# Optimization experiments

Measured on AMD Instinct MI355X. Metric: run time of the kernel, lower is better.

Reference implementation:

```python
import jax, jax.numpy as jnp
import numpy as np

B, S, I, H, L = 64, 1024, 512, 512, 2


def setup_inputs() -> dict:
    key = jax.random.key(0)
    ks = jax.random.split(key, 9)
    stdv = 1.0 / np.sqrt(H)
    u = lambda k, shape: jax.random.uniform(k, shape, jnp.float32, -stdv, stdv)
    return {
        "x": jax.random.normal(ks[0], (B, S, I), jnp.float32),
        "w_ih0": u(ks[1], (3 * H, I)),
        "w_hh0": u(ks[2], (3 * H, H)),
        "b_ih0": u(ks[3], (3 * H,)),
        "b_hh0": u(ks[4], (3 * H,)),
        "w_ih1": u(ks[5], (3 * H, H)),
        "w_hh1": u(ks[6], (3 * H, H)),
        "b_ih1": u(ks[7], (3 * H,)),
        "b_hh1": u(ks[8], (3 * H,)),
    }


def _gru_layer(x_seq, w_ih, w_hh, b_ih, b_hh):
    """x_seq: [S, B, I]. Returns (hs [S, B, H], h_last [B, H])."""
    h = w_hh.shape[1]
    # Precompute all input-to-hidden gate pre-activations in one big GEMM.
    gx_seq = jnp.einsum('sbi,gi->sbg', x_seq, w_ih) + b_ih  # [S, B, 3H]

    def step(h_prev, gx):
        gh = h_prev @ w_hh.T + b_hh  # [B, 3H]
        xr, xz, xn = jnp.split(gx, 3, axis=-1)
        hr, hz, hn = jnp.split(gh, 3, axis=-1)
        r = jax.nn.sigmoid(xr + hr)
        z = jax.nn.sigmoid(xz + hz)
        n = jnp.tanh(xn + r * hn)
        h_new = (1.0 - z) * n + z * h_prev
        return h_new, h_new

    h0 = jnp.zeros((x_seq.shape[1], h), x_seq.dtype)
    h_last, hs = jax.lax.scan(step, h0, gx_seq)
    return hs, h_last


def reference(x, w_ih0, w_hh0, b_ih0, b_hh0, w_ih1, w_hh1, b_ih1, b_hh1):
    xs = jnp.transpose(x, (1, 0, 2))  # [S, B, I] (batch_first -> time-major)
    hs0, h_last0 = _gru_layer(xs, w_ih0, w_hh0, b_ih0, b_hh0)
    hs1, h_last1 = _gru_layer(hs0, w_ih1, w_hh1, b_ih1, b_hh1)
    output = jnp.transpose(hs1, (1, 0, 2))  # [B, S, H]
    h_n = jnp.stack([h_last0, h_last1], axis=0)  # [L, B, H]
    return output, h_n
```

## Files before the change

### kernel.cpp

```cpp
#include <hip/hip_runtime.h>
#include <hip/hip_bf16.h>
#include <cstddef>

typedef __attribute__((ext_vector_type(8))) short bf16x8;
typedef __attribute__((ext_vector_type(4))) float f32x4;
typedef __attribute__((ext_vector_type(4))) unsigned int u32x4;

constexpr int kB = 64;
constexpr int kS = 1024;
constexpr int kH = 512;
constexpr int kNBG = 4;
constexpr int kNUG = 32;
constexpr int kHst = 520;
constexpr unsigned kDone4 = 0x01010101u;
constexpr int kSpinCap = 1 << 16;

__device__ __forceinline__ unsigned short f2bf(float f) {
  unsigned int u = __float_as_uint(f);
  u += 0x7FFFu + ((u >> 16) & 1u);
  return (unsigned short)(u >> 16);
}

__device__ __forceinline__ void st_u32_coh(unsigned int* p, unsigned int v) {
  asm volatile("global_store_dword %0, %1, off sc0 sc1" ::"v"(p), "v"(v) : "memory");
}
__device__ __forceinline__ void st_u64_coh(void* p, unsigned long long v) {
  asm volatile("global_store_dwordx2 %0, %1, off sc0 sc1" ::"v"(p), "v"(v) : "memory");
}
__device__ __forceinline__ void st_flag_release8(unsigned char* p, unsigned int v) {
  asm volatile("s_waitcnt vmcnt(0)\n\tglobal_store_byte %0, %1, off sc0 sc1"
               ::"v"(p), "v"(v) : "memory");
}

#define COH_LD16(dst, p, OFF)                                             \
  asm volatile("global_load_dwordx4 %0, %1, off offset:" #OFF " sc0 sc1"  \
               : "=v"(dst) : "v"(p) : "memory")

__device__ __forceinline__ void wait_vm0(void) {
  asm volatile("s_waitcnt vmcnt(0)" ::: "memory");
  __builtin_amdgcn_sched_barrier(0);
}

__device__ __forceinline__ int poll32(const unsigned char* p) {
  for (int i = 0; i < kSpinCap; ++i) {
    u32x4 a, b;
    asm volatile(
        "global_load_dwordx4 %0, %2, off sc0 sc1\n\t"
        "global_load_dwordx4 %1, %2, off offset:16 sc0 sc1\n\t"
        "s_waitcnt vmcnt(0)"
        : "=v"(a), "=v"(b) : "v"(p) : "memory");
    if (a[0] == kDone4 && a[1] == kDone4 && a[2] == kDone4 && a[3] == kDone4 &&
        b[0] == kDone4 && b[1] == kDone4 && b[2] == kDone4 && b[3] == kDone4)
      return 1;
  }
  return 0;
}

__global__ void init_coh(unsigned int* __restrict__ zbase, int n) {
  int i = blockIdx.x * blockDim.x + threadIdx.x;
  if (i < n) st_u32_coh(zbase + i, 0u);
}

__global__ void cvt_f32_bf16(const float* __restrict__ in,
                             unsigned short* __restrict__ out, int n4) {
  int i = blockIdx.x * blockDim.x + threadIdx.x;
  if (i >= n4) return;
  float4 v = ((const float4*)in)[i];
  ushort4 o;
  o.x = f2bf(v.x); o.y = f2bf(v.y); o.z = f2bf(v.z); o.w = f2bf(v.w);
  ((ushort4*)out)[i] = o;
}

__global__ void cvt_x_t(const float* __restrict__ in,
                        unsigned short* __restrict__ out, int n4) {
  int i4 = blockIdx.x * blockDim.x + threadIdx.x;
  if (i4 >= n4) return;
  int d = i4 * 4;
  int i = d & (kH - 1);
  int rem = d / kH;
  int b = rem & (kB - 1);
  int s = rem / kB;
  float4 v = *(const float4*)(in + ((size_t)b * kS + s) * kH + i);
  ushort4 o;
  o.x = f2bf(v.x); o.y = f2bf(v.y); o.z = f2bf(v.z); o.w = f2bf(v.w);
  *(ushort4*)(out + (size_t)d) = o;
}

__launch_bounds__(256, 1)
__global__ void gru_fused(const unsigned short* __restrict__ xbf,
                          const unsigned short* __restrict__ wih0,
                          const unsigned short* __restrict__ whh0,
                          const unsigned short* __restrict__ wih1,
                          const unsigned short* __restrict__ whh1,
                          const float* __restrict__ bih0, const float* __restrict__ bhh0,
                          const float* __restrict__ bih1, const float* __restrict__ bhh1,
                          unsigned short* __restrict__ hs0,
                          unsigned short* __restrict__ h1buf,
                          unsigned char* __restrict__ f0,
                          unsigned char* __restrict__ f1,
                          float* __restrict__ out) {
  const int tid  = threadIdx.x;
  const int lane = tid & 63;
  const int wv   = tid >> 6;
  const int wgid = blockIdx.x;
  const int layer = wgid >> 7;
  const int bg    = wgid & 3;
  const int ug    = (wgid & 127) >> 2;
  const int bgb0  = bg * 16;
  const int j0w   = ug * 16 + wv * 4;

  const unsigned short* wih = layer ? wih1 : wih0;
  const unsigned short* whh = layer ? whh1 : whh0;
  const float* bih = layer ? bih1 : bih0;
  const float* bhh = layer ? bhh1 : bhh0;

  bf16x8 bx[16], bh[16];
  {
    const int n = lane & 15, hi = lane >> 4;
    if (n < 12) {
      const int orig = (n >> 2) * kH + j0w + (n & 3);
      const unsigned short* pX = wih + (size_t)orig * kH + hi * 8;
      const unsigned short* pH = whh + (size_t)orig * kH + hi * 8;
#pragma unroll
      for (int kk = 0; kk < 16; ++kk) {
        bx[kk] = *(const bf16x8*)(pX + kk * 32);
        bh[kk] = *(const bf16x8*)(pH + kk * 32);
      }
    } else {
      bf16x8 z = {0, 0, 0, 0, 0, 0, 0, 0};
#pragma unroll
      for (int kk = 0; kk < 16; ++kk) { bx[kk] = z; bh[kk] = z; }
    }
  }

  const int gb  = tid & 15;
  const int guu = tid >> 4;
  const int unit = ug * 16 + guu;
  const float bihr = bih[unit], bihz = bih[kH + unit], bihn = bih[2 * kH + unit];
  const float bhhr = bhh[unit], bhhz = bhh[kH + unit], bhhn = bhh[2 * kH + unit];
  float hprev = 0.0f;

  __shared__ unsigned short hA[16][kHst];
  __shared__ unsigned short hX[16][kHst];
  __shared__ float gxl[16][52];
  __shared__ float ghl[16][52];
  __shared__ unsigned short hl[16][20];
  __shared__ float hlf[16][20];

  const int n_  = lane & 15;
  const int ahi = (lane >> 4) * 8;
  const int srow  = lane & 15;
  const int scol0 = wv * 128 + (lane >> 4) * 32;

  unsigned char* myf = (layer ? f1 : f0);

  for (int t = 0; t < kS; ++t) {
    f32x4 accx = {0.f, 0.f, 0.f, 0.f};
    if (layer == 0) {
      const unsigned short* pAX = xbf + ((size_t)t * kB + bgb0 + n_) * kH + ahi;
#pragma unroll
      for (int kk = 0; kk < 16; ++kk) {
        bf16x8 ax = *(const bf16x8*)(pAX + kk * 32);
        accx = __builtin_amdgcn_mfma_f32_16x16x32_bf16(ax, bx[kk], accx, 0, 0, 0);
      }
    }

    int ok = 1;
    if (layer == 0) {
      if (t > 0 && tid == 0) ok = poll32(f0 + ((size_t)(t - 1) * kNBG + bg) * kNUG);
    } else {
      if (tid == 0) ok = poll32(f0 + ((size_t)t * kNBG + bg) * kNUG);
      else if (t > 0 && tid == 64) ok = poll32(f1 + ((size_t)(t - 1) * kNBG + bg) * kNUG);
    }
    if (!__syncthreads_and(ok)) return;

    bf16x8 tA[4], tX[4];
    if (t > 0) {
      const unsigned short* sp =
          ((layer == 0) ? hs0 + ((size_t)(t - 1) * kB + bgb0 + srow) * kH
                        : h1buf + ((size_t)((t - 1) & 1) * kB + bgb0 + srow) * kH) + scol0;
      COH_LD16(tA[0], sp, 0); COH_LD16(tA[1], sp, 16);
      COH_LD16(tA[2], sp, 32); COH_LD16(tA[3], sp, 48);
    }
    if (layer == 1) {
      const unsigned short* sx =
          hs0 + ((size_t)t * kB + bgb0 + srow) * kH + scol0;
      COH_LD16(tX[0], sx, 0); COH_LD16(tX[1], sx, 16);
      COH_LD16(tX[2], sx, 32); COH_LD16(tX[3], sx, 48);
    }
    wait_vm0();
    if (t > 0) {
#pragma unroll
      for (int it = 0; it < 4; ++it)
        *(bf16x8*)&hA[srow][scol0 + it * 8] = tA[it];
    }
    if (layer == 1) {
#pragma unroll
      for (int it = 0; it < 4; ++it)
        *(bf16x8*)&hX[srow][scol0 + it * 8] = tX[it];
    }
    __syncthreads();

    if (layer == 1) {
#pragma unroll
      for (int kk = 0; kk < 16; ++kk) {
        bf16x8 axv = *(const bf16x8*)&hX[n_][kk * 32 + ahi];
        accx = __builtin_amdgcn_mfma_f32_16x16x32_bf16(axv, bx[kk], accx, 0, 0, 0);
      }
    }
    f32x4 acch = {0.f, 0.f, 0.f, 0.f};
    if (t > 0) {
#pragma unroll
      for (int kk = 0; kk < 16; ++kk) {
        bf16x8 ahv = *(const bf16x8*)&hA[n_][kk * 32 + ahi];
        acch = __builtin_amdgcn_mfma_f32_16x16x32_bf16(ahv, bh[kk], acch, 0, 0, 0);
      }
    }
    if (n_ < 12) {
      const int m0 = (lane >> 4) * 4;
#pragma unroll
      for (int r = 0; r < 4; ++r) {
        gxl[m0 + r][wv * 12 + n_] = accx[r];
        ghl[m0 + r][wv * 12 + n_] = acch[r];
      }
    }
    __syncthreads();

    {
      const int c0 = (guu >> 2) * 12, du = guu & 3;
      const float xr = gxl[gb][c0 + du]     + bihr;
      const float xz = gxl[gb][c0 + 4 + du] + bihz;
      const float xn = gxl[gb][c0 + 8 + du] + bihn;
      const float hr = ghl[gb][c0 + du]     + bhhr;
      const float hzv = ghl[gb][c0 + 4 + du] + bhhz;
      const float hn = ghl[gb][c0 + 8 + du] + bhhn;
      const float r = 1.0f / (1.0f + __expf(-(xr + hr)));
      const float z = 1.0f / (1.0f + __expf(-(xz + hzv)));
      const float nn = tanhf(xn + r * hn);
      const float hnew = (1.0f - z) * nn + z * hprev;
      hprev = hnew;
      hl[gb][guu] = f2bf(hnew);
      if (layer == 1) hlf[gb][guu] = hnew;
      if (t == kS - 1)
        out[(size_t)kB * kS * kH + (size_t)layer * kB * kH +
            (size_t)(bgb0 + gb) * kH + unit] = hnew;
    }
    __syncthreads();

    if (tid < 64) {
      const int b = tid >> 2, q = tid & 3;
      unsigned long long pk = *(const unsigned long long*)&hl[b][q * 4];
      if (layer == 0)
        st_u64_coh(hs0 + ((size_t)t * kB + bgb0 + b) * kH + ug * 16 + q * 4, pk);
      else
        st_u64_coh(h1buf + ((size_t)(t & 1) * kB + bgb0 + b) * kH + ug * 16 + q * 4, pk);
    } else if (tid < 128 && layer == 1) {
      const int b = (tid - 64) >> 2, q = (tid - 64) & 3;
      *(float4*)(out + ((size_t)(bgb0 + b) * kS + t) * kH + ug * 16 + q * 4) =
          *(const float4*)&hlf[b][q * 4];
    }
    if (tid == 0)
      st_flag_release8(myf + ((size_t)t * kNBG + bg) * kNUG + ug, 1u);
  }
}

extern "C" void kernel_launch(void* const* d_in, const int* in_sizes, int n_in,
                              void* d_out, int out_size, void* d_ws, size_t ws_size,
                              hipStream_t stream) {
  const float* x     = (const float*)d_in[0];
  const float* w_ih0 = (const float*)d_in[1];
  const float* w_hh0 = (const float*)d_in[2];
  const float* b_ih0 = (const float*)d_in[3];
  const float* b_hh0 = (const float*)d_in[4];
  const float* w_ih1 = (const float*)d_in[5];
  const float* w_hh1 = (const float*)d_in[6];
  const float* b_ih1 = (const float*)d_in[7];
  const float* b_hh1 = (const float*)d_in[8];
  float* out = (float*)d_out;

  unsigned short* ws = (unsigned short*)d_ws;
  const size_t nX = (size_t)kB * kS * kH;
  const size_t nW = (size_t)3 * kH * kH;
  unsigned short* xbf   = ws;
  unsigned short* wih0b = xbf + nX;
  unsigned short* whh0b = wih0b + nW;
  unsigned short* wih1b = whh0b + nW;
  unsigned short* whh1b = wih1b + nW;
  unsigned short* hs0   = whh1b + nW;
  unsigned short* h1buf = hs0 + nX;
  unsigned char*  f0    = (unsigned char*)(h1buf + 2 * kB * kH);
  unsigned char*  f1    = f0 + (size_t)kS * kNBG * kNUG;

  {
    int nz = (int)(2 * (size_t)kS * kNBG * kNUG / 4);
    init_coh<<<(nz + 255) / 256, 256, 0, stream>>>((unsigned int*)f0, nz);
  }
  {
    int n4 = (int)(nX / 4);
    cvt_x_t<<<n4 / 256, 256, 0, stream>>>(x, xbf, n4);
    int w4 = (int)(nW / 4);
    cvt_f32_bf16<<<w4 / 256, 256, 0, stream>>>(w_ih0, wih0b, w4);
    cvt_f32_bf16<<<w4 / 256, 256, 0, stream>>>(w_hh0, whh0b, w4);
    cvt_f32_bf16<<<w4 / 256, 256, 0, stream>>>(w_ih1, wih1b, w4);
    cvt_f32_bf16<<<w4 / 256, 256, 0, stream>>>(w_hh1, whh1b, w4);
  }

  gru_fused<<<dim3(256), dim3(256), 0, stream>>>(
      xbf, wih0b, whh0b, wih1b, whh1b,
      b_ih0, b_hh0, b_ih1, b_hh1,
      hs0, h1buf, f0, f1, out);
}
```

Measured before the change: 5.263 ms.

## Replace flag-based cross-block sync with sentinel-filled data polling

Drops the per-step flag arrays and their release/poll round trips. The hidden-state buffers (hs0 and the fp32 output) are pre-filled with NaN-pattern sentinels, and consumers spin directly on the data loads until no sentinel remains. Layer 1 now reads its recurrent state from the fp32 output instead of a separate bf16 double buffer. This removes one dependent memory round trip per step, but relies on the sentinel never appearing in real data, on tear-free 16-byte visibility, and on two extra full-buffer fill kernels.

```diff
diff --git a/kernel.cpp b/kernel.cpp
--- a/kernel.cpp
+++ b/kernel.cpp
@@ -10,10 +10,10 @@
 constexpr int kS = 1024;
 constexpr int kH = 512;
 constexpr int kNBG = 4;
-constexpr int kNUG = 32;
 constexpr int kHst = 520;
-constexpr unsigned kDone4 = 0x01010101u;
-constexpr int kSpinCap = 1 << 16;
+constexpr unsigned kSentB = 0xFFC0FFC0u;
+constexpr unsigned kSentF = 0xFFC00000u;
+constexpr int kPollCap = 1 << 13;
 
 __device__ __forceinline__ unsigned short f2bf(float f) {
   unsigned int u = __float_as_uint(f);
@@ -21,15 +21,11 @@
   return (unsigned short)(u >> 16);
 }
 
-__device__ __forceinline__ void st_u32_coh(unsigned int* p, unsigned int v) {
-  asm volatile("global_store_dword %0, %1, off sc0 sc1" ::"v"(p), "v"(v) : "memory");
-}
 __device__ __forceinline__ void st_u64_coh(void* p, unsigned long long v) {
   asm volatile("global_store_dwordx2 %0, %1, off sc0 sc1" ::"v"(p), "v"(v) : "memory");
 }
-__device__ __forceinline__ void st_flag_release8(unsigned char* p, unsigned int v) {
-  asm volatile("s_waitcnt vmcnt(0)\n\tglobal_store_byte %0, %1, off sc0 sc1"
-               ::"v"(p), "v"(v) : "memory");
+__device__ __forceinline__ void st_f32x4_coh(void* p, f32x4 v) {
+  asm volatile("global_store_dwordx4 %0, %1, off sc0 sc1" ::"v"(p), "v"(v) : "memory");
 }
 
 #define COH_LD16(dst, p, OFF)                                             \
@@ -41,24 +37,57 @@
   __builtin_amdgcn_sched_barrier(0);
 }
 
-__device__ __forceinline__ int poll32(const unsigned char* p) {
-  for (int i = 0; i < kSpinCap; ++i) {
-    u32x4 a, b;
-    asm volatile(
-        "global_load_dwordx4 %0, %2, off sc0 sc1\n\t"
-        "global_load_dwordx4 %1, %2, off offset:16 sc0 sc1\n\t"
-        "s_waitcnt vmcnt(0)"
-        : "=v"(a), "=v"(b) : "v"(p) : "memory");
-    if (a[0] == kDone4 && a[1] == kDone4 && a[2] == kDone4 && a[3] == kDone4 &&
-        b[0] == kDone4 && b[1] == kDone4 && b[2] == kDone4 && b[3] == kDone4)
+__device__ __forceinline__ int stage_bf16(const unsigned short* sp, bf16x8* tA) {
+  for (int r = 0; r < kPollCap; ++r) {
+    COH_LD16(tA[0], sp, 0);  COH_LD16(tA[1], sp, 16);
+    COH_LD16(tA[2], sp, 32); COH_LD16(tA[3], sp, 48);
+    wait_vm0();
+    int stale = 0;
+#pragma unroll
+    for (int i = 0; i < 4; ++i) {
+      u32x4 w = *(const u32x4*)&tA[i];
+      stale |= (w[0] == kSentB) | (w[1] == kSentB) | (w[2] == kSentB) | (w[3] == kSentB);
+    }
+    if (!stale) return 1;
+  }
+  return 0;
+}
+
+__device__ __forceinline__ bf16x8 pk_bf16(f32x4 lo, f32x4 hi) {
+  union { u32x4 u; bf16x8 h; } r;
+  asm("v_cvt_pk_bf16_f32 %0, %1, %2" : "=v"(r.u[0]) : "v"(lo[0]), "v"(lo[1]));
+  asm("v_cvt_pk_bf16_f32 %0, %1, %2" : "=v"(r.u[1]) : "v"(lo[2]), "v"(lo[3]));
+  asm("v_cvt_pk_bf16_f32 %0, %1, %2" : "=v"(r.u[2]) : "v"(hi[0]), "v"(hi[1]));
+  asm("v_cvt_pk_bf16_f32 %0, %1, %2" : "=v"(r.u[3]) : "v"(hi[2]), "v"(hi[3]));
+  return r.h;
+}
+
+__device__ __forceinline__ int stage_f32(const float* sp, bf16x8* o) {
+  f32x4 v[8];
+  for (int r = 0; r < kPollCap; ++r) {
+    COH_LD16(v[0], sp, 0);   COH_LD16(v[1], sp, 16);
+    COH_LD16(v[2], sp, 32);  COH_LD16(v[3], sp, 48);
+    COH_LD16(v[4], sp, 64);  COH_LD16(v[5], sp, 80);
+    COH_LD16(v[6], sp, 96);  COH_LD16(v[7], sp, 112);
+    wait_vm0();
+    int stale = 0;
+#pragma unroll
+    for (int i = 0; i < 8; ++i) {
+      u32x4 w = *(const u32x4*)&v[i];
+      stale |= (w[0] == kSentF) | (w[1] == kSentF) | (w[2] == kSentF) | (w[3] == kSentF);
+    }
+    if (!stale) {
+#pragma unroll
+      for (int j = 0; j < 4; ++j) o[j] = pk_bf16(v[2 * j], v[2 * j + 1]);
       return 1;
+    }
   }
   return 0;
 }
 
-__global__ void init_coh(unsigned int* __restrict__ zbase, int n) {
+__global__ void fill32(unsigned int* __restrict__ p, unsigned int v, int n) {
   int i = blockIdx.x * blockDim.x + threadIdx.x;
-  if (i < n) st_u32_coh(zbase + i, 0u);
+  if (i < n) p[i] = v;
 }
 
 __global__ void cvt_f32_bf16(const float* __restrict__ in,
@@ -95,9 +124,6 @@
                           const float* __restrict__ bih0, const float* __restrict__ bhh0,
                           const float* __restrict__ bih1, const float* __restrict__ bhh1,
                           unsigned short* __restrict__ hs0,
-                          unsigned short* __restrict__ h1buf,
-                          unsigned char* __restrict__ f0,
-                          unsigned char* __restrict__ f1,
                           float* __restrict__ out) {
   const int tid  = threadIdx.x;
   const int lane = tid & 63;
@@ -151,8 +177,7 @@
   const int ahi = (lane >> 4) * 8;
   const int srow  = lane & 15;
   const int scol0 = wv * 128 + (lane >> 4) * 32;
-
-  unsigned char* myf = (layer ? f1 : f0);
+  const int fseg  = wv * 4 + (lane >> 4);
 
   for (int t = 0; t < kS; ++t) {
     f32x4 accx = {0.f, 0.f, 0.f, 0.f};
@@ -166,40 +191,30 @@
     }
 
     int ok = 1;
-    if (layer == 0) {
-      if (t > 0 && tid == 0) ok = poll32(f0 + ((size_t)(t - 1) * kNBG + bg) * kNUG);
-    } else {
-      if (tid == 0) ok = poll32(f0 + ((size_t)t * kNBG + bg) * kNUG);
-      else if (t > 0 && tid == 64) ok = poll32(f1 + ((size_t)(t - 1) * kNBG + bg) * kNUG);
-    }
-    if (!__syncthreads_and(ok)) return;
-
-    bf16x8 tA[4], tX[4];
     if (t > 0) {
-      const unsigned short* sp =
-          ((layer == 0) ? hs0 + ((size_t)(t - 1) * kB + bgb0 + srow) * kH
-                        : h1buf + ((size_t)((t - 1) & 1) * kB + bgb0 + srow) * kH) + scol0;
-      COH_LD16(tA[0], sp, 0); COH_LD16(tA[1], sp, 16);
-      COH_LD16(tA[2], sp, 32); COH_LD16(tA[3], sp, 48);
+      if (layer == 0) {
+        bf16x8 tA[4];
+        ok &= stage_bf16(hs0 + ((size_t)(t - 1) * kB + bgb0 + srow) * kH + scol0, tA);
+#pragma unroll
+        for (int it = 0; it < 4; ++it)
+          *(bf16x8*)&hA[srow][scol0 + it * 8] = tA[it];
+      } else {
+        bf16x8 tA[4];
+        const float* sp = out + ((size_t)(bgb0 + srow) * kS + (t - 1)) * kH + fseg * 32;
+        ok &= stage_f32(sp, tA);
+#pragma unroll
+        for (int it = 0; it < 4; ++it)
+          *(bf16x8*)&hA[srow][fseg * 32 + it * 8] = tA[it];
+      }
     }
     if (layer == 1) {
-      const unsigned short* sx =
-          hs0 + ((size_t)t * kB + bgb0 + srow) * kH + scol0;
-      COH_LD16(tX[0], sx, 0); COH_LD16(tX[1], sx, 16);
-      COH_LD16(tX[2], sx, 32); COH_LD16(tX[3], sx, 48);
-    }
-    wait_vm0();
-    if (t > 0) {
-#pragma unroll
-      for (int it = 0; it < 4; ++it)
-        *(bf16x8*)&hA[srow][scol0 + it * 8] = tA[it];
-    }
-    if (layer == 1) {
+      bf16x8 tX[4];
+      ok &= stage_bf16(hs0 + ((size_t)t * kB + bgb0 + srow) * kH + scol0, tX);
 #pragma unroll
       for (int it = 0; it < 4; ++it)
         *(bf16x8*)&hX[srow][scol0 + it * 8] = tX[it];
     }
-    __syncthreads();
+    if (!__syncthreads_and(ok)) return;
 
     if (layer == 1) {
 #pragma unroll
@@ -247,20 +262,19 @@
     }
     __syncthreads();
 
-    if (tid < 64) {
-      const int b = tid >> 2, q = tid & 3;
-      unsigned long long pk = *(const unsigned long long*)&hl[b][q * 4];
-      if (layer == 0)
+    if (layer == 0) {
+      if (tid < 64) {
+        const int b = tid >> 2, q = tid & 3;
+        unsigned long long pk = *(const unsigned long long*)&hl[b][q * 4];
         st_u64_coh(hs0 + ((size_t)t * kB + bgb0 + b) * kH + ug * 16 + q * 4, pk);
-      else
-        st_u64_coh(h1buf + ((size_t)(t & 1) * kB + bgb0 + b) * kH + ug * 16 + q * 4, pk);
-    } else if (tid < 128 && layer == 1) {
-      const int b = (tid - 64) >> 2, q = (tid - 64) & 3;
-      *(float4*)(out + ((size_t)(bgb0 + b) * kS + t) * kH + ug * 16 + q * 4) =
-          *(const float4*)&hlf[b][q * 4];
-    }
-    if (tid == 0)
-      st_flag_release8(myf + ((size_t)t * kNBG + bg) * kNUG + ug, 1u);
+      }
+    } else {
+      if (tid < 64) {
+        const int b = tid >> 2, q = tid & 3;
+        st_f32x4_coh(out + ((size_t)(bgb0 + b) * kS + t) * kH + ug * 16 + q * 4,
+                     *(const f32x4*)&hlf[b][q * 4]);
+      }
+    }
   }
 }
 
@@ -287,13 +301,12 @@
   unsigned short* wih1b = whh0b + nW;
   unsigned short* whh1b = wih1b + nW;
   unsigned short* hs0   = whh1b + nW;
-  unsigned short* h1buf = hs0 + nX;
-  unsigned char*  f0    = (unsigned char*)(h1buf + 2 * kB * kH);
-  unsigned char*  f1    = f0 + (size_t)kS * kNBG * kNUG;
 
   {
-    int nz = (int)(2 * (size_t)kS * kNBG * kNUG / 4);
-    init_coh<<<(nz + 255) / 256, 256, 0, stream>>>((unsigned int*)f0, nz);
+    int nh = (int)(nX / 2);
+    fill32<<<(nh + 255) / 256, 256, 0, stream>>>((unsigned int*)hs0, kSentB, nh);
+    int no = (int)nX;
+    fill32<<<(no + 255) / 256, 256, 0, stream>>>((unsigned int*)out, kSentF, no);
   }
   {
     int n4 = (int)(nX / 4);
@@ -308,5 +321,5 @@
   gru_fused<<<dim3(256), dim3(256), 0, stream>>>(
       xbf, wih0b, whh0b, wih1b, whh1b,
       b_ih0, b_hh0, b_ih1, b_hh1,
-      hs0, h1buf, f0, f1, out);
-}
+      hs0, out);
+}
```

Result: slower. 6.144 ms (+16.7%).

## Compute GRU gates in registers via shuffles and use per-wave completion flags

Applied to the files above, without the earlier changes.

Removes the shared-memory round trip for gate pre-activations: lanes gather z and n gate values with cross-lane shuffles and compute hnew directly from the MFMA accumulators. This drops two block barriers per timestep. Each wave now stores its own bf16 hidden outputs and publishes a per-wave flag, and a whole wave polls the 128 flags. The next timestep's layer-0 x operands are prefetched into registers after the flag store so they overlap the wait. The trade-offs are many small 16-bit coherent stores, a 4x larger flag array, and higher register pressure from the prefetched operands.

```diff
diff --git a/kernel.cpp b/kernel.cpp
--- a/kernel.cpp
+++ b/kernel.cpp
@@ -24,34 +24,36 @@
 __device__ __forceinline__ void st_u32_coh(unsigned int* p, unsigned int v) {
   asm volatile("global_store_dword %0, %1, off sc0 sc1" ::"v"(p), "v"(v) : "memory");
 }
-__device__ __forceinline__ void st_u64_coh(void* p, unsigned long long v) {
-  asm volatile("global_store_dwordx2 %0, %1, off sc0 sc1" ::"v"(p), "v"(v) : "memory");
-}
-__device__ __forceinline__ void st_flag_release8(unsigned char* p, unsigned int v) {
-  asm volatile("s_waitcnt vmcnt(0)\n\tglobal_store_byte %0, %1, off sc0 sc1"
-               ::"v"(p), "v"(v) : "memory");
+__device__ __forceinline__ void st_u16_coh(unsigned short* p, unsigned int v) {
+  asm volatile("global_store_short %0, %1, off sc0 sc1" ::"v"(p), "v"(v) : "memory");
+}
+__device__ __forceinline__ void st_u8_coh(unsigned char* p, unsigned int v) {
+  asm volatile("global_store_byte %0, %1, off sc0 sc1" ::"v"(p), "v"(v) : "memory");
 }
 
 #define COH_LD16(dst, p, OFF)                                             \
   asm volatile("global_load_dwordx4 %0, %1, off offset:" #OFF " sc0 sc1"  \
                : "=v"(dst) : "v"(p) : "memory")
+#define CA_LD16(dst, p, OFF)                                              \
+  asm volatile("global_load_dwordx4 %0, %1, off offset:" #OFF              \
+               : "=v"(dst) : "v"(p) : "memory")
 
 __device__ __forceinline__ void wait_vm0(void) {
   asm volatile("s_waitcnt vmcnt(0)" ::: "memory");
   __builtin_amdgcn_sched_barrier(0);
 }
-
-__device__ __forceinline__ int poll32(const unsigned char* p) {
+__device__ __forceinline__ void wait_vm4(void) {
+  asm volatile("s_waitcnt vmcnt(4)" ::: "memory");
+  __builtin_amdgcn_sched_barrier(0);
+}
+
+__device__ __forceinline__ int wave_poll128(const unsigned char* p, int lane) {
+  const unsigned int* pw = (const unsigned int*)p + (lane & 31);
   for (int i = 0; i < kSpinCap; ++i) {
-    u32x4 a, b;
-    asm volatile(
-        "global_load_dwordx4 %0, %2, off sc0 sc1\n\t"
-        "global_load_dwordx4 %1, %2, off offset:16 sc0 sc1\n\t"
-        "s_waitcnt vmcnt(0)"
-        : "=v"(a), "=v"(b) : "v"(p) : "memory");
-    if (a[0] == kDone4 && a[1] == kDone4 && a[2] == kDone4 && a[3] == kDone4 &&
-        b[0] == kDone4 && b[1] == kDone4 && b[2] == kDone4 && b[3] == kDone4)
-      return 1;
+    unsigned int v;
+    asm volatile("global_load_dword %0, %1, off sc0 sc1\n\ts_waitcnt vmcnt(0)"
+                 : "=v"(v) : "v"(pw) : "memory");
+    if (__all((lane < 32) ? (int)(v == kDone4) : 1)) return 1;
   }
   return 0;
 }
@@ -133,134 +135,166 @@
     }
   }
 
-  const int gb  = tid & 15;
-  const int guu = tid >> 4;
-  const int unit = ug * 16 + guu;
-  const float bihr = bih[unit], bihz = bih[kH + unit], bihn = bih[2 * kH + unit];
-  const float bhhr = bhh[unit], bhhz = bhh[kH + unit], bhhn = bhh[2 * kH + unit];
-  float hprev = 0.0f;
+  const int n_   = lane & 15;
+  const int hi_  = lane >> 4;
+  const int ahi  = hi_ * 8;
+  const int m0   = hi_ * 4;
+  const int srow = n_;
+  const int scol0 = wv * 128 + hi_ * 32;
+  const int jj    = lane & 3;
+  const int src_z = (lane & 48) + jj + 4;
+  const int src_n = (lane & 48) + jj + 8;
+  const int u     = j0w + jj;
+
+  const float bihr = bih[u], bihz = bih[kH + u], bihn = bih[2 * kH + u];
+  const float bhhr = bhh[u], bhhz = bhh[kH + u], bhhn = bhh[2 * kH + u];
+  f32x4 hprev = {0.f, 0.f, 0.f, 0.f};
 
   __shared__ unsigned short hA[16][kHst];
   __shared__ unsigned short hX[16][kHst];
-  __shared__ float gxl[16][52];
-  __shared__ float ghl[16][52];
-  __shared__ unsigned short hl[16][20];
-  __shared__ float hlf[16][20];
-
-  const int n_  = lane & 15;
-  const int ahi = (lane >> 4) * 8;
-  const int srow  = lane & 15;
-  const int scol0 = wv * 128 + (lane >> 4) * 32;
-
-  unsigned char* myf = (layer ? f1 : f0);
+
+  unsigned char* myf = layer ? f1 : f0;
+
+  bf16x8 axr[16];
+  if (layer == 0) {
+    const unsigned short* p = xbf + ((size_t)0 * kB + bgb0 + n_) * kH + ahi;
+    CA_LD16(axr[0],  p, 0);   CA_LD16(axr[1],  p, 64);  CA_LD16(axr[2],  p, 128);
+    CA_LD16(axr[3],  p, 192); CA_LD16(axr[4],  p, 256); CA_LD16(axr[5],  p, 320);
+    CA_LD16(axr[6],  p, 384); CA_LD16(axr[7],  p, 448); CA_LD16(axr[8],  p, 512);
+    CA_LD16(axr[9],  p, 576); CA_LD16(axr[10], p, 640); CA_LD16(axr[11], p, 704);
+    CA_LD16(axr[12], p, 768); CA_LD16(axr[13], p, 832); CA_LD16(axr[14], p, 896);
+    CA_LD16(axr[15], p, 960);
+  }
 
   for (int t = 0; t < kS; ++t) {
-    f32x4 accx = {0.f, 0.f, 0.f, 0.f};
-    if (layer == 0) {
-      const unsigned short* pAX = xbf + ((size_t)t * kB + bgb0 + n_) * kH + ahi;
-#pragma unroll
-      for (int kk = 0; kk < 16; ++kk) {
-        bf16x8 ax = *(const bf16x8*)(pAX + kk * 32);
-        accx = __builtin_amdgcn_mfma_f32_16x16x32_bf16(ax, bx[kk], accx, 0, 0, 0);
-      }
-    }
-
     int ok = 1;
     if (layer == 0) {
-      if (t > 0 && tid == 0) ok = poll32(f0 + ((size_t)(t - 1) * kNBG + bg) * kNUG);
+      if (t > 0 && wv == 0)
+        ok = wave_poll128(f0 + ((size_t)(t - 1) * kNBG + bg) * (kNUG * 4), lane);
     } else {
-      if (tid == 0) ok = poll32(f0 + ((size_t)t * kNBG + bg) * kNUG);
-      else if (t > 0 && tid == 64) ok = poll32(f1 + ((size_t)(t - 1) * kNBG + bg) * kNUG);
+      if (wv == 0)
+        ok = wave_poll128(f0 + ((size_t)t * kNBG + bg) * (kNUG * 4), lane);
+      else if (t > 0 && wv == 1)
+        ok = wave_poll128(f1 + ((size_t)(t - 1) * kNBG + bg) * (kNUG * 4), lane);
     }
     if (!__syncthreads_and(ok)) return;
 
     bf16x8 tA[4], tX[4];
     if (t > 0) {
       const unsigned short* sp =
-          ((layer == 0) ? hs0 + ((size_t)(t - 1) * kB + bgb0 + srow) * kH
-                        : h1buf + ((size_t)((t - 1) & 1) * kB + bgb0 + srow) * kH) + scol0;
-      COH_LD16(tA[0], sp, 0); COH_LD16(tA[1], sp, 16);
+          (layer == 0) ? hs0 + ((size_t)(t - 1) * kB + bgb0 + srow) * kH + scol0
+                       : h1buf + ((size_t)((t - 1) & 1) * kB + bgb0 + srow) * kH + scol0;
+      COH_LD16(tA[0], sp, 0);  COH_LD16(tA[1], sp, 16);
       COH_LD16(tA[2], sp, 32); COH_LD16(tA[3], sp, 48);
     }
     if (layer == 1) {
-      const unsigned short* sx =
-          hs0 + ((size_t)t * kB + bgb0 + srow) * kH + scol0;
-      COH_LD16(tX[0], sx, 0); COH_LD16(tX[1], sx, 16);
+      const unsigned short* sx = hs0 + ((size_t)t * kB + bgb0 + srow) * kH + scol0;
+      COH_LD16(tX[0], sx, 0);  COH_LD16(tX[1], sx, 16);
       COH_LD16(tX[2], sx, 32); COH_LD16(tX[3], sx, 48);
     }
-    wait_vm0();
-    if (t > 0) {
-#pragma unroll
-      for (int it = 0; it < 4; ++it)
-        *(bf16x8*)&hA[srow][scol0 + it * 8] = tA[it];
-    }
-    if (layer == 1) {
+
+    f32x4 accx = {0.f, 0.f, 0.f, 0.f};
+    f32x4 acch = {0.f, 0.f, 0.f, 0.f};
+
+    if (layer == 0) {
+      if (t > 0) wait_vm4(); else wait_vm0();
+#pragma unroll
+      for (int kk = 0; kk < 16; ++kk)
+        accx = __builtin_amdgcn_mfma_f32_16x16x32_bf16(axr[kk], bx[kk], accx, 0, 0, 0);
+      wait_vm0();
+      if (t > 0) {
+#pragma unroll
+        for (int it = 0; it < 4; ++it)
+          *(bf16x8*)&hA[srow][scol0 + it * 8] = tA[it];
+      }
+      __syncthreads();
+      if (t > 0) {
+#pragma unroll
+        for (int kk = 0; kk < 16; ++kk) {
+          bf16x8 ahv = *(const bf16x8*)&hA[n_][kk * 32 + ahi];
+          acch = __builtin_amdgcn_mfma_f32_16x16x32_bf16(ahv, bh[kk], acch, 0, 0, 0);
+        }
+      }
+    } else {
+      wait_vm0();
 #pragma unroll
       for (int it = 0; it < 4; ++it)
         *(bf16x8*)&hX[srow][scol0 + it * 8] = tX[it];
-    }
-    __syncthreads();
-
-    if (layer == 1) {
+      if (t > 0) {
+#pragma unroll
+        for (int it = 0; it < 4; ++it)
+          *(bf16x8*)&hA[srow][scol0 + it * 8] = tA[it];
+      }
+      __syncthreads();
 #pragma unroll
       for (int kk = 0; kk < 16; ++kk) {
         bf16x8 axv = *(const bf16x8*)&hX[n_][kk * 32 + ahi];
         accx = __builtin_amdgcn_mfma_f32_16x16x32_bf16(axv, bx[kk], accx, 0, 0, 0);
       }
-    }
-    f32x4 acch = {0.f, 0.f, 0.f, 0.f};
-    if (t > 0) {
-#pragma unroll
-      for (int kk = 0; kk < 16; ++kk) {
-        bf16x8 ahv = *(const bf16x8*)&hA[n_][kk * 32 + ahi];
-        acch = __builtin_amdgcn_mfma_f32_16x16x32_bf16(ahv, bh[kk], acch, 0, 0, 0);
-      }
-    }
-    if (n_ < 12) {
-      const int m0 = (lane >> 4) * 4;
+      if (t > 0) {
+#pragma unroll
+        for (int kk = 0; kk < 16; ++kk) {
+          bf16x8 ahv = *(const bf16x8*)&hA[n_][kk * 32 + ahi];
+          acch = __builtin_amdgcn_mfma_f32_16x16x32_bf16(ahv, bh[kk], acch, 0, 0, 0);
+        }
+      }
+    }
+
+    f32x4 xz_, xn_, hz_, hn_;
+#pragma unroll
+    for (int r = 0; r < 4; ++r) {
+      xz_[r] = __shfl(accx[r], src_z, 64);
+      xn_[r] = __shfl(accx[r], src_n, 64);
+      hz_[r] = __shfl(acch[r], src_z, 64);
+      hn_[r] = __shfl(acch[r], src_n, 64);
+    }
+    f32x4 hnew;
+#pragma unroll
+    for (int r = 0; r < 4; ++r) {
+      const float xr = accx[r] + bihr;
+      const float xz = xz_[r] + bihz;
+      const float xn = xn_[r] + bihn;
+      const float hr = acch[r] + bhhr;
+      const float hzv = hz_[r] + bhhz;
+      const float hnv = hn_[r] + bhhn;
+      const float rr = 1.0f / (1.0f + __expf(-(xr + hr)));
+      const float zz = 1.0f / (1.0f + __expf(-(xz + hzv)));
+      const float nn = tanhf(xn + rr * hnv);
+      hnew[r] = (1.0f - zz) * nn + zz * hprev[r];
+    }
+    hprev = hnew;
+
+    if (n_ < 4) {
 #pragma unroll
       for (int r = 0; r < 4; ++r) {
-        gxl[m0 + r][wv * 12 + n_] = accx[r];
-        ghl[m0 + r][wv * 12 + n_] = acch[r];
-      }
-    }
-    __syncthreads();
-
-    {
-      const int c0 = (guu >> 2) * 12, du = guu & 3;
-      const float xr = gxl[gb][c0 + du]     + bihr;
-      const float xz = gxl[gb][c0 + 4 + du] + bihz;
-      const float xn = gxl[gb][c0 + 8 + du] + bihn;
-      const float hr = ghl[gb][c0 + du]     + bhhr;
-      const float hzv = ghl[gb][c0 + 4 + du] + bhhz;
-      const float hn = ghl[gb][c0 + 8 + du] + bhhn;
-      const float r = 1.0f / (1.0f + __expf(-(xr + hr)));
-      const float z = 1.0f / (1.0f + __expf(-(xz + hzv)));
-      const float nn = tanhf(xn + r * hn);
-      const float hnew = (1.0f - z) * nn + z * hprev;
-      hprev = hnew;
-      hl[gb][guu] = f2bf(hnew);
-      if (layer == 1) hlf[gb][guu] = hnew;
-      if (t == kS - 1)
-        out[(size_t)kB * kS * kH + (size_t)layer * kB * kH +
-            (size_t)(bgb0 + gb) * kH + unit] = hnew;
-    }
-    __syncthreads();
-
-    if (tid < 64) {
-      const int b = tid >> 2, q = tid & 3;
-      unsigned long long pk = *(const unsigned long long*)&hl[b][q * 4];
-      if (layer == 0)
-        st_u64_coh(hs0 + ((size_t)t * kB + bgb0 + b) * kH + ug * 16 + q * 4, pk);
-      else
-        st_u64_coh(h1buf + ((size_t)(t & 1) * kB + bgb0 + b) * kH + ug * 16 + q * 4, pk);
-    } else if (tid < 128 && layer == 1) {
-      const int b = (tid - 64) >> 2, q = (tid - 64) & 3;
-      *(float4*)(out + ((size_t)(bgb0 + b) * kS + t) * kH + ug * 16 + q * 4) =
-          *(const float4*)&hlf[b][q * 4];
-    }
-    if (tid == 0)
-      st_flag_release8(myf + ((size_t)t * kNBG + bg) * kNUG + ug, 1u);
+        const unsigned int hv = f2bf(hnew[r]);
+        if (layer == 0) {
+          st_u16_coh(hs0 + ((size_t)t * kB + bgb0 + m0 + r) * kH + u, hv);
+        } else {
+          st_u16_coh(h1buf + ((size_t)(t & 1) * kB + bgb0 + m0 + r) * kH + u, hv);
+          out[((size_t)(bgb0 + m0 + r) * kS + t) * kH + u] = hnew[r];
+        }
+      }
+      if (t == kS - 1) {
+#pragma unroll
+        for (int r = 0; r < 4; ++r)
+          out[(size_t)kB * kS * kH + (size_t)layer * kB * kH +
+              (size_t)(bgb0 + m0 + r) * kH + u] = hnew[r];
+      }
+    }
+    asm volatile("s_waitcnt vmcnt(0)" ::: "memory");
+    if (lane == 0)
+      st_u8_coh(myf + ((size_t)t * kNBG + bg) * (kNUG * 4) + ug * 4 + wv, 1u);
+
+    if (layer == 0 && t + 1 < kS) {
+      const unsigned short* p = xbf + ((size_t)(t + 1) * kB + bgb0 + n_) * kH + ahi;
+      CA_LD16(axr[0],  p, 0);   CA_LD16(axr[1],  p, 64);  CA_LD16(axr[2],  p, 128);
+      CA_LD16(axr[3],  p, 192); CA_LD16(axr[4],  p, 256); CA_LD16(axr[5],  p, 320);
+      CA_LD16(axr[6],  p, 384); CA_LD16(axr[7],  p, 448); CA_LD16(axr[8],  p, 512);
+      CA_LD16(axr[9],  p, 576); CA_LD16(axr[10], p, 640); CA_LD16(axr[11], p, 704);
+      CA_LD16(axr[12], p, 768); CA_LD16(axr[13], p, 832); CA_LD16(axr[14], p, 896);
+      CA_LD16(axr[15], p, 960);
+    }
   }
 }
 
@@ -289,10 +323,10 @@
   unsigned short* hs0   = whh1b + nW;
   unsigned short* h1buf = hs0 + nX;
   unsigned char*  f0    = (unsigned char*)(h1buf + 2 * kB * kH);
-  unsigned char*  f1    = f0 + (size_t)kS * kNBG * kNUG;
+  unsigned char*  f1    = f0 + (size_t)kS * kNBG * kNUG * 4;
 
   {
-    int nz = (int)(2 * (size_t)kS * kNBG * kNUG / 4);
+    int nz = (int)(2 * (size_t)kS * kNBG * kNUG * 4 / 4);
     init_coh<<<(nz + 255) / 256, 256, 0, stream>>>((unsigned int*)f0, nz);
   }
   {
```

After: 7.745 ms. 1.47x slower.

## Co-schedule both GRU layers in one workgroup with wavefront skew and x prefetch

Applied to the files above, without the earlier changes.

Each workgroup now runs layer 0 at step e and layer 1 at step e-1 together, so the launch drops from 256 to 128 workgroups and only one flag array and one poll per step remain. Layer 0's hidden state at e-1 is loaded once and used both for layer 0's recurrent GEMM and layer 1's input GEMM. The x tile for the next step is prefetched into registers so its load overlaps the flag wait. In exchange each workgroup holds four weight slices in registers, which raises register pressure and may spill. It also does two gate computations per step, so the per-step critical path gets longer.

```diff
diff --git a/kernel.cpp b/kernel.cpp
--- a/kernel.cpp
+++ b/kernel.cpp
@@ -27,17 +27,27 @@
 __device__ __forceinline__ void st_u64_coh(void* p, unsigned long long v) {
   asm volatile("global_store_dwordx2 %0, %1, off sc0 sc1" ::"v"(p), "v"(v) : "memory");
 }
-__device__ __forceinline__ void st_flag_release8(unsigned char* p, unsigned int v) {
-  asm volatile("s_waitcnt vmcnt(0)\n\tglobal_store_byte %0, %1, off sc0 sc1"
-               ::"v"(p), "v"(v) : "memory");
+__device__ __forceinline__ void st_u8_coh(unsigned char* p, unsigned int v) {
+  asm volatile("global_store_byte %0, %1, off sc0 sc1" ::"v"(p), "v"(v) : "memory");
 }
 
 #define COH_LD16(dst, p, OFF)                                             \
   asm volatile("global_load_dwordx4 %0, %1, off offset:" #OFF " sc0 sc1"  \
                : "=v"(dst) : "v"(p) : "memory")
+#define CA_LD16(dst, p, OFF)                                              \
+  asm volatile("global_load_dwordx4 %0, %1, off offset:" #OFF              \
+               : "=v"(dst) : "v"(p) : "memory")
 
 __device__ __forceinline__ void wait_vm0(void) {
   asm volatile("s_waitcnt vmcnt(0)" ::: "memory");
+  __builtin_amdgcn_sched_barrier(0);
+}
+__device__ __forceinline__ void wait_vm4(void) {
+  asm volatile("s_waitcnt vmcnt(4)" ::: "memory");
+  __builtin_amdgcn_sched_barrier(0);
+}
+__device__ __forceinline__ void wait_vm8(void) {
+  asm volatile("s_waitcnt vmcnt(8)" ::: "memory");
   __builtin_amdgcn_sched_barrier(0);
 }
 
@@ -96,171 +106,205 @@
                           const float* __restrict__ bih1, const float* __restrict__ bhh1,
                           unsigned short* __restrict__ hs0,
                           unsigned short* __restrict__ h1buf,
-                          unsigned char* __restrict__ f0,
-                          unsigned char* __restrict__ f1,
+                          unsigned char* __restrict__ flags,
                           float* __restrict__ out) {
   const int tid  = threadIdx.x;
   const int lane = tid & 63;
   const int wv   = tid >> 6;
   const int wgid = blockIdx.x;
-  const int layer = wgid >> 7;
-  const int bg    = wgid & 3;
-  const int ug    = (wgid & 127) >> 2;
-  const int bgb0  = bg * 16;
-  const int j0w   = ug * 16 + wv * 4;
-
-  const unsigned short* wih = layer ? wih1 : wih0;
-  const unsigned short* whh = layer ? whh1 : whh0;
-  const float* bih = layer ? bih1 : bih0;
-  const float* bhh = layer ? bhh1 : bhh0;
-
-  bf16x8 bx[16], bh[16];
+  const int bg   = wgid & 3;
+  const int ug   = wgid >> 2;
+  const int bgb0 = bg * 16;
+  const int j0w  = ug * 16 + wv * 4;
+
+  bf16x8 bx0[16], bh0f[16], bx1[16], bh1f[16];
   {
     const int n = lane & 15, hi = lane >> 4;
     if (n < 12) {
       const int orig = (n >> 2) * kH + j0w + (n & 3);
-      const unsigned short* pX = wih + (size_t)orig * kH + hi * 8;
-      const unsigned short* pH = whh + (size_t)orig * kH + hi * 8;
+      const unsigned short* p0x = wih0 + (size_t)orig * kH + hi * 8;
+      const unsigned short* p0h = whh0 + (size_t)orig * kH + hi * 8;
+      const unsigned short* p1x = wih1 + (size_t)orig * kH + hi * 8;
+      const unsigned short* p1h = whh1 + (size_t)orig * kH + hi * 8;
 #pragma unroll
       for (int kk = 0; kk < 16; ++kk) {
-        bx[kk] = *(const bf16x8*)(pX + kk * 32);
-        bh[kk] = *(const bf16x8*)(pH + kk * 32);
+        bx0[kk]  = *(const bf16x8*)(p0x + kk * 32);
+        bh0f[kk] = *(const bf16x8*)(p0h + kk * 32);
+        bx1[kk]  = *(const bf16x8*)(p1x + kk * 32);
+        bh1f[kk] = *(const bf16x8*)(p1h + kk * 32);
       }
     } else {
       bf16x8 z = {0, 0, 0, 0, 0, 0, 0, 0};
 #pragma unroll
-      for (int kk = 0; kk < 16; ++kk) { bx[kk] = z; bh[kk] = z; }
+      for (int kk = 0; kk < 16; ++kk) { bx0[kk] = z; bh0f[kk] = z; bx1[kk] = z; bh1f[kk] = z; }
     }
   }
 
   const int gb  = tid & 15;
   const int guu = tid >> 4;
   const int unit = ug * 16 + guu;
-  const float bihr = bih[unit], bihz = bih[kH + unit], bihn = bih[2 * kH + unit];
-  const float bhhr = bhh[unit], bhhz = bhh[kH + unit], bhhn = bhh[2 * kH + unit];
-  float hprev = 0.0f;
+  const float b0r = bih0[unit], b0z = bih0[kH + unit], b0n = bih0[2 * kH + unit];
+  const float h0r = bhh0[unit], h0z = bhh0[kH + unit], h0n = bhh0[2 * kH + unit];
+  const float b1r = bih1[unit], b1z = bih1[kH + unit], b1n = bih1[2 * kH + unit];
+  const float h1r = bhh1[unit], h1z = bhh1[kH + unit], h1n = bhh1[2 * kH + unit];
+  float hprev0 = 0.0f, hprev1 = 0.0f;
 
   __shared__ unsigned short hA[16][kHst];
-  __shared__ unsigned short hX[16][kHst];
-  __shared__ float gxl[16][52];
-  __shared__ float ghl[16][52];
-  __shared__ unsigned short hl[16][20];
+  __shared__ unsigned short hB[16][kHst];
+  __shared__ float gx0l[16][52], gh0l[16][52];
+  __shared__ float gx1l[16][52], gh1l[16][52];
+  __shared__ unsigned short hl0[16][20], hl1[16][20];
   __shared__ float hlf[16][20];
 
   const int n_  = lane & 15;
-  const int ahi = (lane >> 4) * 8;
-  const int srow  = lane & 15;
-  const int scol0 = wv * 128 + (lane >> 4) * 32;
-
-  unsigned char* myf = (layer ? f1 : f0);
-
-  for (int t = 0; t < kS; ++t) {
-    f32x4 accx = {0.f, 0.f, 0.f, 0.f};
-    if (layer == 0) {
-      const unsigned short* pAX = xbf + ((size_t)t * kB + bgb0 + n_) * kH + ahi;
-#pragma unroll
-      for (int kk = 0; kk < 16; ++kk) {
-        bf16x8 ax = *(const bf16x8*)(pAX + kk * 32);
-        accx = __builtin_amdgcn_mfma_f32_16x16x32_bf16(ax, bx[kk], accx, 0, 0, 0);
-      }
-    }
-
+  const int hi_ = lane >> 4;
+  const int ahi = hi_ * 8;
+  const int srow = n_;
+  const int scol0 = wv * 128 + hi_ * 32;
+
+  bf16x8 axr[16];
+  {
+    const unsigned short* p = xbf + ((size_t)0 * kB + bgb0 + n_) * kH + ahi;
+    CA_LD16(axr[0],  p, 0);   CA_LD16(axr[1],  p, 64);  CA_LD16(axr[2],  p, 128);
+    CA_LD16(axr[3],  p, 192); CA_LD16(axr[4],  p, 256); CA_LD16(axr[5],  p, 320);
+    CA_LD16(axr[6],  p, 384); CA_LD16(axr[7],  p, 448); CA_LD16(axr[8],  p, 512);
+    CA_LD16(axr[9],  p, 576); CA_LD16(axr[10], p, 640); CA_LD16(axr[11], p, 704);
+    CA_LD16(axr[12], p, 768); CA_LD16(axr[13], p, 832); CA_LD16(axr[14], p, 896);
+    CA_LD16(axr[15], p, 960);
+  }
+
+  for (int e = 0; e <= kS; ++e) {
     int ok = 1;
-    if (layer == 0) {
-      if (t > 0 && tid == 0) ok = poll32(f0 + ((size_t)(t - 1) * kNBG + bg) * kNUG);
-    } else {
-      if (tid == 0) ok = poll32(f0 + ((size_t)t * kNBG + bg) * kNUG);
-      else if (t > 0 && tid == 64) ok = poll32(f1 + ((size_t)(t - 1) * kNBG + bg) * kNUG);
-    }
+    if (e >= 1 && tid == 0)
+      ok = poll32(flags + ((size_t)(e - 1) * kNBG + bg) * kNUG);
     if (!__syncthreads_and(ok)) return;
 
-    bf16x8 tA[4], tX[4];
-    if (t > 0) {
-      const unsigned short* sp =
-          ((layer == 0) ? hs0 + ((size_t)(t - 1) * kB + bgb0 + srow) * kH
-                        : h1buf + ((size_t)((t - 1) & 1) * kB + bgb0 + srow) * kH) + scol0;
-      COH_LD16(tA[0], sp, 0); COH_LD16(tA[1], sp, 16);
+    bf16x8 tA[4], tB[4];
+    if (e >= 1) {
+      const unsigned short* sp = hs0 + ((size_t)(e - 1) * kB + bgb0 + srow) * kH + scol0;
+      COH_LD16(tA[0], sp, 0);  COH_LD16(tA[1], sp, 16);
       COH_LD16(tA[2], sp, 32); COH_LD16(tA[3], sp, 48);
     }
-    if (layer == 1) {
-      const unsigned short* sx =
-          hs0 + ((size_t)t * kB + bgb0 + srow) * kH + scol0;
-      COH_LD16(tX[0], sx, 0); COH_LD16(tX[1], sx, 16);
-      COH_LD16(tX[2], sx, 32); COH_LD16(tX[3], sx, 48);
-    }
-    wait_vm0();
-    if (t > 0) {
+    if (e >= 2) {
+      const unsigned short* sb = h1buf + ((size_t)((e - 2) & 1) * kB + bgb0 + srow) * kH + scol0;
+      COH_LD16(tB[0], sb, 0);  COH_LD16(tB[1], sb, 16);
+      COH_LD16(tB[2], sb, 32); COH_LD16(tB[3], sb, 48);
+    }
+
+    f32x4 ax0 = {0,0,0,0}, ah0 = {0,0,0,0}, ax1 = {0,0,0,0}, ah1 = {0,0,0,0};
+    if (e < kS) {
+      if (e >= 2) wait_vm8(); else if (e == 1) wait_vm4(); else wait_vm0();
+#pragma unroll
+      for (int kk = 0; kk < 16; ++kk)
+        ax0 = __builtin_amdgcn_mfma_f32_16x16x32_bf16(axr[kk], bx0[kk], ax0, 0, 0, 0);
+    }
+
+    if (e >= 1) {
+      wait_vm0();
 #pragma unroll
       for (int it = 0; it < 4; ++it)
         *(bf16x8*)&hA[srow][scol0 + it * 8] = tA[it];
-    }
-    if (layer == 1) {
-#pragma unroll
-      for (int it = 0; it < 4; ++it)
-        *(bf16x8*)&hX[srow][scol0 + it * 8] = tX[it];
+      if (e >= 2) {
+#pragma unroll
+        for (int it = 0; it < 4; ++it)
+          *(bf16x8*)&hB[srow][scol0 + it * 8] = tB[it];
+      }
     }
     __syncthreads();
 
-    if (layer == 1) {
+    if (e >= 1) {
 #pragma unroll
       for (int kk = 0; kk < 16; ++kk) {
-        bf16x8 axv = *(const bf16x8*)&hX[n_][kk * 32 + ahi];
-        accx = __builtin_amdgcn_mfma_f32_16x16x32_bf16(axv, bx[kk], accx, 0, 0, 0);
-      }
-    }
-    f32x4 acch = {0.f, 0.f, 0.f, 0.f};
-    if (t > 0) {
-#pragma unroll
-      for (int kk = 0; kk < 16; ++kk) {
-        bf16x8 ahv = *(const bf16x8*)&hA[n_][kk * 32 + ahi];
-        acch = __builtin_amdgcn_mfma_f32_16x16x32_bf16(ahv, bh[kk], acch, 0, 0, 0);
+        bf16x8 av = *(const bf16x8*)&hA[n_][kk * 32 + ahi];
+        if (e < kS)
+          ah0 = __builtin_amdgcn_mfma_f32_16x16x32_bf16(av, bh0f[kk], ah0, 0, 0, 0);
+        ax1 = __builtin_amdgcn_mfma_f32_16x16x32_bf16(av, bx1[kk], ax1, 0, 0, 0);
+      }
+      if (e >= 2) {
+#pragma unroll
+        for (int kk = 0; kk < 16; ++kk) {
+          bf16x8 bv = *(const bf16x8*)&hB[n_][kk * 32 + ahi];
+          ah1 = __builtin_amdgcn_mfma_f32_16x16x32_bf16(bv, bh1f[kk], ah1, 0, 0, 0);
+        }
       }
     }
     if (n_ < 12) {
-      const int m0 = (lane >> 4) * 4;
+      const int m0 = hi_ * 4;
 #pragma unroll
       for (int r = 0; r < 4; ++r) {
-        gxl[m0 + r][wv * 12 + n_] = accx[r];
-        ghl[m0 + r][wv * 12 + n_] = acch[r];
+        gx0l[m0 + r][wv * 12 + n_] = ax0[r];
+        gh0l[m0 + r][wv * 12 + n_] = ah0[r];
+        gx1l[m0 + r][wv * 12 + n_] = ax1[r];
+        gh1l[m0 + r][wv * 12 + n_] = ah1[r];
       }
     }
     __syncthreads();
 
     {
       const int c0 = (guu >> 2) * 12, du = guu & 3;
-      const float xr = gxl[gb][c0 + du]     + bihr;
-      const float xz = gxl[gb][c0 + 4 + du] + bihz;
-      const float xn = gxl[gb][c0 + 8 + du] + bihn;
-      const float hr = ghl[gb][c0 + du]     + bhhr;
-      const float hzv = ghl[gb][c0 + 4 + du] + bhhz;
-      const float hn = ghl[gb][c0 + 8 + du] + bhhn;
-      const float r = 1.0f / (1.0f + __expf(-(xr + hr)));
-      const float z = 1.0f / (1.0f + __expf(-(xz + hzv)));
-      const float nn = tanhf(xn + r * hn);
-      const float hnew = (1.0f - z) * nn + z * hprev;
-      hprev = hnew;
-      hl[gb][guu] = f2bf(hnew);
-      if (layer == 1) hlf[gb][guu] = hnew;
-      if (t == kS - 1)
-        out[(size_t)kB * kS * kH + (size_t)layer * kB * kH +
-            (size_t)(bgb0 + gb) * kH + unit] = hnew;
+      if (e < kS) {
+        const float xr = gx0l[gb][c0 + du]     + b0r;
+        const float xz = gx0l[gb][c0 + 4 + du] + b0z;
+        const float xn = gx0l[gb][c0 + 8 + du] + b0n;
+        const float hr = gh0l[gb][c0 + du]     + h0r;
+        const float hz = gh0l[gb][c0 + 4 + du] + h0z;
+        const float hn = gh0l[gb][c0 + 8 + du] + h0n;
+        const float r = 1.0f / (1.0f + __expf(-(xr + hr)));
+        const float z = 1.0f / (1.0f + __expf(-(xz + hz)));
+        const float nv = tanhf(xn + r * hn);
+        const float hnew = (1.0f - z) * nv + z * hprev0;
+        hprev0 = hnew;
+        hl0[gb][guu] = f2bf(hnew);
+        if (e == kS - 1)
+          out[(size_t)kB * kS * kH + (size_t)(bgb0 + gb) * kH + unit] = hnew;
+      }
+      if (e >= 1) {
+        const float xr = gx1l[gb][c0 + du]     + b1r;
+        const float xz = gx1l[gb][c0 + 4 + du] + b1z;
+        const float xn = gx1l[gb][c0 + 8 + du] + b1n;
+        const float hr = gh1l[gb][c0 + du]     + h1r;
+        const float hz = gh1l[gb][c0 + 4 + du] + h1z;
+        const float hn = gh1l[gb][c0 + 8 + du] + h1n;
+        const float r = 1.0f / (1.0f + __expf(-(xr + hr)));
+        const float z = 1.0f / (1.0f + __expf(-(xz + hz)));
+        const float nv = tanhf(xn + r * hn);
+        const float hnew = (1.0f - z) * nv + z * hprev1;
+        hprev1 = hnew;
+        hl1[gb][guu] = f2bf(hnew);
+        hlf[gb][guu] = hnew;
+        if (e == kS)
+          out[(size_t)kB * kS * kH + (size_t)kB * kH + (size_t)(bgb0 + gb) * kH + unit] = hnew;
+      }
     }
     __syncthreads();
 
     if (tid < 64) {
       const int b = tid >> 2, q = tid & 3;
-      unsigned long long pk = *(const unsigned long long*)&hl[b][q * 4];
-      if (layer == 0)
-        st_u64_coh(hs0 + ((size_t)t * kB + bgb0 + b) * kH + ug * 16 + q * 4, pk);
-      else
-        st_u64_coh(h1buf + ((size_t)(t & 1) * kB + bgb0 + b) * kH + ug * 16 + q * 4, pk);
-    } else if (tid < 128 && layer == 1) {
+      if (e < kS)
+        st_u64_coh(hs0 + ((size_t)e * kB + bgb0 + b) * kH + ug * 16 + q * 4,
+                   *(const unsigned long long*)&hl0[b][q * 4]);
+      if (e >= 1)
+        st_u64_coh(h1buf + ((size_t)((e - 1) & 1) * kB + bgb0 + b) * kH + ug * 16 + q * 4,
+                   *(const unsigned long long*)&hl1[b][q * 4]);
+    } else if (tid < 128 && e >= 1) {
       const int b = (tid - 64) >> 2, q = (tid - 64) & 3;
-      *(float4*)(out + ((size_t)(bgb0 + b) * kS + t) * kH + ug * 16 + q * 4) =
+      *(float4*)(out + ((size_t)(bgb0 + b) * kS + (e - 1)) * kH + ug * 16 + q * 4) =
           *(const float4*)&hlf[b][q * 4];
     }
-    if (tid == 0)
-      st_flag_release8(myf + ((size_t)t * kNBG + bg) * kNUG + ug, 1u);
+    if (tid == 0 && e < kS) {
+      asm volatile("s_waitcnt vmcnt(0)" ::: "memory");
+      st_u8_coh(flags + ((size_t)e * kNBG + bg) * kNUG + ug, 1u);
+    }
+
+    if (e + 1 < kS) {
+      const unsigned short* p = xbf + ((size_t)(e + 1) * kB + bgb0 + n_) * kH + ahi;
+      CA_LD16(axr[0],  p, 0);   CA_LD16(axr[1],  p, 64);  CA_LD16(axr[2],  p, 128);
+      CA_LD16(axr[3],  p, 192); CA_LD16(axr[4],  p, 256); CA_LD16(axr[5],  p, 320);
+      CA_LD16(axr[6],  p, 384); CA_LD16(axr[7],  p, 448); CA_LD16(axr[8],  p, 512);
+      CA_LD16(axr[9],  p, 576); CA_LD16(axr[10], p, 640); CA_LD16(axr[11], p, 704);
+      CA_LD16(axr[12], p, 768); CA_LD16(axr[13], p, 832); CA_LD16(axr[14], p, 896);
+      CA_LD16(axr[15], p, 960);
+    }
   }
 }
 
@@ -288,12 +332,11 @@
   unsigned short* whh1b = wih1b + nW;
   unsigned short* hs0   = whh1b + nW;
   unsigned short* h1buf = hs0 + nX;
-  unsigned char*  f0    = (unsigned char*)(h1buf + 2 * kB * kH);
-  unsigned char*  f1    = f0 + (size_t)kS * kNBG * kNUG;
+  unsigned char*  flags = (unsigned char*)(h1buf + 2 * kB * kH);
 
   {
-    int nz = (int)(2 * (size_t)kS * kNBG * kNUG / 4);
-    init_coh<<<(nz + 255) / 256, 256, 0, stream>>>((unsigned int*)f0, nz);
+    int nz = (int)((size_t)kS * kNBG * kNUG / 4);
+    init_coh<<<(nz + 255) / 256, 256, 0, stream>>>((unsigned int*)flags, nz);
   }
   {
     int n4 = (int)(nX / 4);
@@ -305,8 +348,8 @@
     cvt_f32_bf16<<<w4 / 256, 256, 0, stream>>>(w_hh1, whh1b, w4);
   }
 
-  gru_fused<<<dim3(256), dim3(256), 0, stream>>>(
+  gru_fused<<<dim3(kNBG * kNUG), dim3(256), 0, stream>>>(
       xbf, wih0b, whh0b, wih1b, whh1b,
       b_ih0, b_hh0, b_ih1, b_hh1,
-      hs0, h1buf, f0, f1, out);
-}
+      hs0, h1buf, flags, out);
+}
```

Result: slower. 6.839 ms (+29.9%).
